# Performance work log

Measured on AMD Instinct MI355X. Metric: run time of the kernel, lower is better.

Reference implementation:

```python
import jax, jax.numpy as jnp
import numpy as np

EPS = 1e-06

def _feature_map(x):
    # elu(x) + 1, positive feature map
    return jax.nn.elu(x) + 1.0

def setup_inputs() -> dict:
    key = jax.random.key(0)
    k1, k2, k3 = jax.random.split(key, 3)
    B, L, d_k, d_v = 2, 4096, 128, 128
    Q = jax.random.normal(k1, (B, L, d_k), dtype=jnp.float32)
    K = jax.random.normal(k2, (B, L, d_k), dtype=jnp.float32)
    V = jax.random.normal(k3, (B, L, d_v), dtype=jnp.float32)
    return {"Q": Q, "K": K, "V": V}

def reference(Q, K, V):
    # Causal linear attention (ELU feature map).
    # out_l = phi(Q_l) @ sum_{j<=l} phi(K_j)^T V_j
    # Z_l   = phi(Q_l) . sum_{j<=l} phi(K_j)
    phiQ = _feature_map(Q)                       # (B, L, dk)
    phiK = _feature_map(K)                       # (B, L, dk)
    # cumulative KV state: (B, L, dk, dv) -- parallel replacement of the
    # original per-step bmm loop
    KV = jnp.cumsum(phiK[..., :, None] * V[..., None, :], axis=1)
    out = jnp.einsum('blk,blkv->blv', phiQ, KV)  # (B, L, dv)
    Kc = jnp.cumsum(phiK, axis=1)                # (B, L, dk)
    Z = jnp.einsum('blk,blk->bl', phiQ, Kc)[..., None]  # (B, L, 1)
    return out / (Z + EPS)
```

## Files before the change

### kernel.cpp

```cpp
#include <hip/hip_runtime.h>


#define EPS 1e-6f

constexpr int Bc = 2;
constexpr int L  = 4096;
constexpr int D  = 128;
constexpr int C  = 128;
constexpr int NC = L / C;
constexpr int P  = 136;

typedef short sh8 __attribute__((ext_vector_type(8)));
typedef float f4  __attribute__((ext_vector_type(4)));

__device__ __forceinline__ float phi(float x) {
    return x > 0.0f ? x + 1.0f : __expf(x);
}
__device__ __forceinline__ unsigned short f2bf(float f) {
    unsigned u = __float_as_uint(f);
    unsigned r = (u + 0x7FFFu + ((u >> 16) & 1u)) >> 16;
    return (unsigned short)r;
}
__device__ __forceinline__ float bf2f(unsigned short h) {
    return __uint_as_float(((unsigned)h) << 16);
}

__global__ __launch_bounds__(256) void k1(
    const float* __restrict__ K, const float* __restrict__ V,
    unsigned short* __restrict__ SB, float* __restrict__ Ksum) {
    const int c = blockIdx.x, b = blockIdx.y, vs = blockIdx.z;
    const int tid = threadIdx.x;
    __shared__ __align__(16) unsigned short sA[64 * P];
    __shared__ __align__(16) unsigned short sB[128 * P];
    const size_t base = ((size_t)b * L + (size_t)c * C) * D;

    for (int k = 0; k < 8; ++k) {
        int fi = tid + 256 * k;
        int l = fi & 127, v4 = fi >> 7;
        float4 vd = *(const float4*)(V + base + (size_t)l * D + vs * 64 + v4 * 4);
        sA[(v4 * 4 + 0) * P + l] = f2bf(vd.x);
        sA[(v4 * 4 + 1) * P + l] = f2bf(vd.y);
        sA[(v4 * 4 + 2) * P + l] = f2bf(vd.z);
        sA[(v4 * 4 + 3) * P + l] = f2bf(vd.w);
    }
    for (int k = 0; k < 16; ++k) {
        int fi = tid + 256 * k;
        int l = fi & 127, i4 = fi >> 7;
        float4 kd = *(const float4*)(K + base + (size_t)l * D + i4 * 4);
        sB[(i4 * 4 + 0) * P + l] = f2bf(phi(kd.x));
        sB[(i4 * 4 + 1) * P + l] = f2bf(phi(kd.y));
        sB[(i4 * 4 + 2) * P + l] = f2bf(phi(kd.z));
        sB[(i4 * 4 + 3) * P + l] = f2bf(phi(kd.w));
    }
    __syncthreads();

    if (vs == 0 && tid < 128) {
        const unsigned* row = (const unsigned*)(sB + tid * P);
        float s = 0.0f;
        for (int j = 0; j < 64; ++j) {
            unsigned d = row[(tid + j) & 63];
            s += bf2f((unsigned short)(d & 0xffff)) + bf2f((unsigned short)(d >> 16));
        }
        Ksum[((size_t)(b * NC + c)) * D + tid] = s;
    }

    const int w = tid >> 6, lane = tid & 63;
    const int r = lane & 15, q = lane >> 4;
    f4 acc[8];
#pragma unroll
    for (int f = 0; f < 8; ++f) acc[f] = {0.f, 0.f, 0.f, 0.f};
#pragma unroll
    for (int ks = 0; ks < 4; ++ks) {
        sh8 a = *(const sh8*)(sA + (w * 16 + r) * P + ks * 32 + q * 8);
#pragma unroll
        for (int f = 0; f < 8; ++f) {
            sh8 bb = *(const sh8*)(sB + (f * 16 + r) * P + ks * 32 + q * 8);
            acc[f] = __builtin_amdgcn_mfma_f32_16x16x32_bf16(a, bb, acc[f], 0, 0, 0);
        }
    }
    unsigned short* out = SB + ((size_t)(b * NC + c)) * D * D;
#pragma unroll
    for (int f = 0; f < 8; ++f) {
        int i = f * 16 + r;
#pragma unroll
        for (int e = 0; e < 4; ++e) {
            int v = vs * 64 + w * 16 + q * 4 + e;
            out[(size_t)v * D + i] = f2bf(acc[f][e]);
        }
    }
}

__global__ __launch_bounds__(256) void k_scan(unsigned short* __restrict__ SB,
                                              float* __restrict__ Ksum) {
    const int SD = D * D;
    int idx = blockIdx.x * 256 + threadIdx.x;
    if (idx < Bc * SD) {
        int b = idx / SD, e = idx % SD;
        float run = 0.0f;
        for (int c = 0; c < NC; ++c) {
            size_t off = ((size_t)(b * NC + c)) * SD + e;
            float t = bf2f(SB[off]);
            SB[off]  = f2bf(run);
            run += t;
        }
    } else if (idx < Bc * SD + Bc * D) {
        int rr = idx - Bc * SD;
        int b = rr >> 7, i = rr & 127;
        float run = 0.0f;
        for (int c = 0; c < NC; ++c) {
            size_t off = ((size_t)(b * NC + c)) * D + i;
            float t = Ksum[off];
            Ksum[off] = run;
            run += t;
        }
    }
}

__global__ __launch_bounds__(256) void k_out(
    const float* __restrict__ Q, const float* __restrict__ K,
    const float* __restrict__ V, const unsigned short* __restrict__ SB,
    const float* __restrict__ Ksum, float* __restrict__ Out) {
    const int c = blockIdx.x, b = blockIdx.y, rs = blockIdx.z;
    const int tid = threadIdx.x;
    __shared__ __align__(16) unsigned short sQ[32 * P];
    __shared__ __align__(16) unsigned short sB[128 * P];
    __shared__ __align__(16) unsigned short sAm[32 * P];
    __shared__ float sKp[128];
    __shared__ float sZ[32];
    const size_t base  = ((size_t)b * L + (size_t)c * C) * D;
    const size_t qbase = base + (size_t)rs * 32 * D;

    for (int k = 0; k < 4; ++k) {
        int fi = tid + 256 * k;
        int row = fi >> 5, c4 = fi & 31;
        float4 qd = *(const float4*)(Q + qbase + (size_t)row * D + c4 * 4);
        uint2 pk;
        pk.x = (unsigned)f2bf(phi(qd.x)) | ((unsigned)f2bf(phi(qd.y)) << 16);
        pk.y = (unsigned)f2bf(phi(qd.z)) | ((unsigned)f2bf(phi(qd.w)) << 16);
        *(uint2*)(sQ + row * P + c4 * 4) = pk;
    }
    for (int k = 0; k < 16; ++k) {
        int fi = tid + 256 * k;
        int row = fi >> 5, c4 = fi & 31;
        float4 kd = *(const float4*)(K + base + (size_t)row * D + c4 * 4);
        uint2 pk;
        pk.x = (unsigned)f2bf(phi(kd.x)) | ((unsigned)f2bf(phi(kd.y)) << 16);
        pk.y = (unsigned)f2bf(phi(kd.z)) | ((unsigned)f2bf(phi(kd.w)) << 16);
        *(uint2*)(sB + row * P + c4 * 4) = pk;
    }
    if (tid < 128) sKp[tid] = Ksum[((size_t)(b * NC + c)) * D + tid];
    __syncthreads();

    const int w = tid >> 6, lane = tid & 63;
    const int r = lane & 15, q = lane >> 4;
    const int rbase = (w & 1) * 16;
    const int cbase = (w >> 1) * 64;

    f4 a2[4];
#pragma unroll
    for (int f = 0; f < 4; ++f) a2[f] = {0.f, 0.f, 0.f, 0.f};
#pragma unroll
    for (int ks = 0; ks < 4; ++ks) {
        sh8 a = *(const sh8*)(sQ + (rbase + r) * P + ks * 32 + q * 8);
#pragma unroll
        for (int f = 0; f < 4; ++f) {
            sh8 bb = *(const sh8*)(sB + (cbase + f * 16 + r) * P + ks * 32 + q * 8);
            a2[f] = __builtin_amdgcn_mfma_f32_16x16x32_bf16(a, bb, a2[f], 0, 0, 0);
        }
    }
#pragma unroll
    for (int f = 0; f < 4; ++f) {
        int j = cbase + f * 16 + r;
#pragma unroll
        for (int e = 0; e < 4; ++e) {
            int lr = rbase + q * 4 + e;
            float vv = (j <= rs * 32 + lr) ? a2[f][e] : 0.0f;
            sAm[lr * P + j] = f2bf(vv);
        }
    }
    __syncthreads();

    for (int k = 0; k < 16; ++k) {
        int fi = tid + 256 * k;
        int j = fi & 127, v4 = fi >> 7;
        float4 vd = *(const float4*)(V + base + (size_t)j * D + v4 * 4);
        sB[(v4 * 4 + 0) * P + j] = f2bf(vd.x);
        sB[(v4 * 4 + 1) * P + j] = f2bf(vd.y);
        sB[(v4 * 4 + 2) * P + j] = f2bf(vd.z);
        sB[(v4 * 4 + 3) * P + j] = f2bf(vd.w);
    }
    if (tid < 32) {
        const unsigned* am = (const unsigned*)(sAm + tid * P);
        const unsigned* qq = (const unsigned*)(sQ + tid * P);
        float zi = 0.0f, zn = 0.0f;
        for (int j = 0; j < 64; ++j) {
            int jj = (tid + j) & 63;
            unsigned da = am[jj];
            zi += bf2f((unsigned short)(da & 0xffff)) + bf2f((unsigned short)(da >> 16));
            unsigned dq = qq[jj];
            zn += bf2f((unsigned short)(dq & 0xffff)) * sKp[2 * jj]
                + bf2f((unsigned short)(dq >> 16))    * sKp[2 * jj + 1];
        }
        sZ[tid] = zi + zn + EPS;
    }
    __syncthreads();

    f4 acc[4];
#pragma unroll
    for (int f = 0; f < 4; ++f) acc[f] = {0.f, 0.f, 0.f, 0.f};
#pragma unroll
    for (int ks = 0; ks < 4; ++ks) {
        sh8 a = *(const sh8*)(sAm + (rbase + r) * P + ks * 32 + q * 8);
#pragma unroll
        for (int f = 0; f < 4; ++f) {
            sh8 bb = *(const sh8*)(sB + (cbase + f * 16 + r) * P + ks * 32 + q * 8);
            acc[f] = __builtin_amdgcn_mfma_f32_16x16x32_bf16(a, bb, acc[f], 0, 0, 0);
        }
    }
    __syncthreads();

    const uint4* sbg = (const uint4*)(SB + ((size_t)(b * NC + c)) * D * D);
    for (int k = 0; k < 8; ++k) {
        int fi = tid + 256 * k;
        int v = fi >> 4, ch = fi & 15;
        uint4 dd = sbg[fi];
        *(uint4*)(sB + v * P + ch * 8) = dd;
    }
    __syncthreads();

#pragma unroll
    for (int ks = 0; ks < 4; ++ks) {
        sh8 a = *(const sh8*)(sQ + (rbase + r) * P + ks * 32 + q * 8);
#pragma unroll
        for (int f = 0; f < 4; ++f) {
            sh8 bb = *(const sh8*)(sB + (cbase + f * 16 + r) * P + ks * 32 + q * 8);
            acc[f] = __builtin_amdgcn_mfma_f32_16x16x32_bf16(a, bb, acc[f], 0, 0, 0);
        }
    }

#pragma unroll
    for (int f = 0; f < 4; ++f) {
        int v = cbase + f * 16 + r;
#pragma unroll
        for (int e = 0; e < 4; ++e) {
            int lr = rbase + q * 4 + e;
            Out[base + (size_t)(rs * 32 + lr) * D + v] = acc[f][e] / sZ[lr];
        }
    }
}

extern "C" void kernel_launch(void* const* d_in, const int* in_sizes, int n_in,
                              void* d_out, int out_size, void* d_ws, size_t ws_size,
                              hipStream_t stream) {
    const float* Q = (const float*)d_in[0];
    const float* K = (const float*)d_in[1];
    const float* V = (const float*)d_in[2];
    float* Out = (float*)d_out;
    unsigned short* SB = (unsigned short*)d_ws;
    float* Ksum = (float*)((char*)d_ws + (size_t)Bc * NC * D * D * 2);

    k1<<<dim3(NC, Bc, 2), 256, 0, stream>>>(K, V, SB, Ksum);
    int total = Bc * D * D + Bc * D;
    k_scan<<<dim3((total + 255) / 256), 256, 0, stream>>>(SB, Ksum);
    k_out<<<dim3(NC, Bc, 4), 256, 0, stream>>>(Q, K, V, SB, Ksum, Out);
}
```

Before: 84.13 us.

## Fold K-sum and normalizer reductions into MFMA via ones-row augmentation, use 512 threads

Instead of summing rows serially with a few threads, both kernels append a row of ones (and the prefix K-sum row) to the shared operand tiles, so the normalizer and K-sums come out of extra MFMA tiles computed by designated waves. Blocks grow to 512 threads with each wave owning a smaller output tile, and k_out loads V up front into a separate buffer, removing a barrier and a serialized reload phase. This trades more shared memory per block, and K-sum and Z now computed with bf16 operands (Ksum rounded to bf16), for removal of the single-thread reduction loops.

```diff
diff --git a/kernel.cpp b/kernel.cpp
--- a/kernel.cpp
+++ b/kernel.cpp
@@ -18,24 +18,23 @@
 }
 __device__ __forceinline__ unsigned short f2bf(float f) {
     unsigned u = __float_as_uint(f);
-    unsigned r = (u + 0x7FFFu + ((u >> 16) & 1u)) >> 16;
-    return (unsigned short)r;
+    return (unsigned short)((u + 0x7FFFu + ((u >> 16) & 1u)) >> 16);
 }
 __device__ __forceinline__ float bf2f(unsigned short h) {
     return __uint_as_float(((unsigned)h) << 16);
 }
 
-__global__ __launch_bounds__(256) void k1(
+__global__ __launch_bounds__(512) void k1(
     const float* __restrict__ K, const float* __restrict__ V,
     unsigned short* __restrict__ SB, float* __restrict__ Ksum) {
     const int c = blockIdx.x, b = blockIdx.y, vs = blockIdx.z;
     const int tid = threadIdx.x;
-    __shared__ __align__(16) unsigned short sA[64 * P];
-    __shared__ __align__(16) unsigned short sB[128 * P];
+    __shared__ __align__(16) unsigned short sA[80 * P];
+    __shared__ __align__(16) unsigned short sKb[128 * P];
     const size_t base = ((size_t)b * L + (size_t)c * C) * D;
 
-    for (int k = 0; k < 8; ++k) {
-        int fi = tid + 256 * k;
+    for (int k = 0; k < 4; ++k) {
+        int fi = tid + 512 * k;
         int l = fi & 127, v4 = fi >> 7;
         float4 vd = *(const float4*)(V + base + (size_t)l * D + vs * 64 + v4 * 4);
         sA[(v4 * 4 + 0) * P + l] = f2bf(vd.x);
@@ -43,50 +42,56 @@
         sA[(v4 * 4 + 2) * P + l] = f2bf(vd.z);
         sA[(v4 * 4 + 3) * P + l] = f2bf(vd.w);
     }
-    for (int k = 0; k < 16; ++k) {
-        int fi = tid + 256 * k;
+    for (int k = 0; k < 2; ++k) {
+        int fi = tid + 512 * k;
+        int row = fi >> 6, colp = fi & 63;
+        *(unsigned*)(sA + (64 + row) * P + colp * 2) = (row == 0) ? 0x3F803F80u : 0u;
+    }
+    for (int k = 0; k < 8; ++k) {
+        int fi = tid + 512 * k;
         int l = fi & 127, i4 = fi >> 7;
         float4 kd = *(const float4*)(K + base + (size_t)l * D + i4 * 4);
-        sB[(i4 * 4 + 0) * P + l] = f2bf(phi(kd.x));
-        sB[(i4 * 4 + 1) * P + l] = f2bf(phi(kd.y));
-        sB[(i4 * 4 + 2) * P + l] = f2bf(phi(kd.z));
-        sB[(i4 * 4 + 3) * P + l] = f2bf(phi(kd.w));
-    }
-    __syncthreads();
-
-    if (vs == 0 && tid < 128) {
-        const unsigned* row = (const unsigned*)(sB + tid * P);
-        float s = 0.0f;
-        for (int j = 0; j < 64; ++j) {
-            unsigned d = row[(tid + j) & 63];
-            s += bf2f((unsigned short)(d & 0xffff)) + bf2f((unsigned short)(d >> 16));
-        }
-        Ksum[((size_t)(b * NC + c)) * D + tid] = s;
-    }
+        sKb[(i4 * 4 + 0) * P + l] = f2bf(phi(kd.x));
+        sKb[(i4 * 4 + 1) * P + l] = f2bf(phi(kd.y));
+        sKb[(i4 * 4 + 2) * P + l] = f2bf(phi(kd.z));
+        sKb[(i4 * 4 + 3) * P + l] = f2bf(phi(kd.w));
+    }
+    __syncthreads();
 
     const int w = tid >> 6, lane = tid & 63;
     const int r = lane & 15, q = lane >> 4;
-    f4 acc[8];
-#pragma unroll
-    for (int f = 0; f < 8; ++f) acc[f] = {0.f, 0.f, 0.f, 0.f};
-#pragma unroll
-    for (int ks = 0; ks < 4; ++ks) {
-        sh8 a = *(const sh8*)(sA + (w * 16 + r) * P + ks * 32 + q * 8);
-#pragma unroll
-        for (int f = 0; f < 8; ++f) {
-            sh8 bb = *(const sh8*)(sB + (f * 16 + r) * P + ks * 32 + q * 8);
+    const int rbase = (w & 3) * 16;
+    const int cbase = (w >> 2) * 64;
+    const bool doZ = (vs == 0) && ((w & 3) == 0);
+
+    f4 acc[4], kz[4];
+#pragma unroll
+    for (int f = 0; f < 4; ++f) { acc[f] = {0.f,0.f,0.f,0.f}; kz[f] = {0.f,0.f,0.f,0.f}; }
+#pragma unroll
+    for (int ks = 0; ks < 4; ++ks) {
+        sh8 a  = *(const sh8*)(sA + (rbase + r) * P + ks * 32 + q * 8);
+        sh8 az = *(const sh8*)(sA + (64 + r) * P + ks * 32 + q * 8);
+#pragma unroll
+        for (int f = 0; f < 4; ++f) {
+            sh8 bb = *(const sh8*)(sKb + (cbase + f * 16 + r) * P + ks * 32 + q * 8);
             acc[f] = __builtin_amdgcn_mfma_f32_16x16x32_bf16(a, bb, acc[f], 0, 0, 0);
+            if (doZ) kz[f] = __builtin_amdgcn_mfma_f32_16x16x32_bf16(az, bb, kz[f], 0, 0, 0);
         }
     }
     unsigned short* out = SB + ((size_t)(b * NC + c)) * D * D;
 #pragma unroll
-    for (int f = 0; f < 8; ++f) {
-        int i = f * 16 + r;
+    for (int f = 0; f < 4; ++f) {
+        int i = cbase + f * 16 + r;
 #pragma unroll
         for (int e = 0; e < 4; ++e) {
-            int v = vs * 64 + w * 16 + q * 4 + e;
+            int v = vs * 64 + rbase + q * 4 + e;
             out[(size_t)v * D + i] = f2bf(acc[f][e]);
         }
+    }
+    if (doZ && q == 0) {
+#pragma unroll
+        for (int f = 0; f < 4; ++f)
+            Ksum[((size_t)(b * NC + c)) * D + cbase + f * 16 + r] = kz[f][0];
     }
 }
 
@@ -116,22 +121,22 @@
     }
 }
 
-__global__ __launch_bounds__(256) void k_out(
+__global__ __launch_bounds__(512) void k_out(
     const float* __restrict__ Q, const float* __restrict__ K,
     const float* __restrict__ V, const unsigned short* __restrict__ SB,
     const float* __restrict__ Ksum, float* __restrict__ Out) {
     const int c = blockIdx.x, b = blockIdx.y, rs = blockIdx.z;
     const int tid = threadIdx.x;
     __shared__ __align__(16) unsigned short sQ[32 * P];
-    __shared__ __align__(16) unsigned short sB[128 * P];
+    __shared__ __align__(16) unsigned short sKb[144 * P];
+    __shared__ __align__(16) unsigned short sV[144 * P];
     __shared__ __align__(16) unsigned short sAm[32 * P];
-    __shared__ float sKp[128];
     __shared__ float sZ[32];
     const size_t base  = ((size_t)b * L + (size_t)c * C) * D;
     const size_t qbase = base + (size_t)rs * 32 * D;
 
-    for (int k = 0; k < 4; ++k) {
-        int fi = tid + 256 * k;
+    for (int k = 0; k < 2; ++k) {
+        int fi = tid + 512 * k;
         int row = fi >> 5, c4 = fi & 31;
         float4 qd = *(const float4*)(Q + qbase + (size_t)row * D + c4 * 4);
         uint2 pk;
@@ -139,92 +144,99 @@
         pk.y = (unsigned)f2bf(phi(qd.z)) | ((unsigned)f2bf(phi(qd.w)) << 16);
         *(uint2*)(sQ + row * P + c4 * 4) = pk;
     }
-    for (int k = 0; k < 16; ++k) {
-        int fi = tid + 256 * k;
+    for (int k = 0; k < 8; ++k) {
+        int fi = tid + 512 * k;
         int row = fi >> 5, c4 = fi & 31;
         float4 kd = *(const float4*)(K + base + (size_t)row * D + c4 * 4);
         uint2 pk;
         pk.x = (unsigned)f2bf(phi(kd.x)) | ((unsigned)f2bf(phi(kd.y)) << 16);
         pk.y = (unsigned)f2bf(phi(kd.z)) | ((unsigned)f2bf(phi(kd.w)) << 16);
-        *(uint2*)(sB + row * P + c4 * 4) = pk;
-    }
-    if (tid < 128) sKp[tid] = Ksum[((size_t)(b * NC + c)) * D + tid];
+        *(uint2*)(sKb + row * P + c4 * 4) = pk;
+    }
+    for (int k = 0; k < 8; ++k) {
+        int fi = tid + 512 * k;
+        int j = fi & 127, v4 = fi >> 7;
+        float4 vd = *(const float4*)(V + base + (size_t)j * D + v4 * 4);
+        sV[(v4 * 4 + 0) * P + j] = f2bf(vd.x);
+        sV[(v4 * 4 + 1) * P + j] = f2bf(vd.y);
+        sV[(v4 * 4 + 2) * P + j] = f2bf(vd.z);
+        sV[(v4 * 4 + 3) * P + j] = f2bf(vd.w);
+    }
+    for (int k = 0; k < 2; ++k) {
+        int fi = tid + 512 * k;
+        int row = fi >> 6, colp = fi & 63;
+        *(unsigned*)(sV + (128 + row) * P + colp * 2) = (row == 0) ? 0x3F803F80u : 0u;
+    }
     __syncthreads();
 
     const int w = tid >> 6, lane = tid & 63;
     const int r = lane & 15, q = lane >> 4;
     const int rbase = (w & 1) * 16;
-    const int cbase = (w >> 1) * 64;
-
-    f4 a2[4];
-#pragma unroll
-    for (int f = 0; f < 4; ++f) a2[f] = {0.f, 0.f, 0.f, 0.f};
+    const int cq = w >> 1, cbase = cq * 32;
+    const bool doZ = (cq == 3);
+
+    f4 a2[2];
+#pragma unroll
+    for (int f = 0; f < 2; ++f) a2[f] = {0.f,0.f,0.f,0.f};
 #pragma unroll
     for (int ks = 0; ks < 4; ++ks) {
         sh8 a = *(const sh8*)(sQ + (rbase + r) * P + ks * 32 + q * 8);
 #pragma unroll
-        for (int f = 0; f < 4; ++f) {
-            sh8 bb = *(const sh8*)(sB + (cbase + f * 16 + r) * P + ks * 32 + q * 8);
+        for (int f = 0; f < 2; ++f) {
+            sh8 bb = *(const sh8*)(sKb + (cbase + f * 16 + r) * P + ks * 32 + q * 8);
             a2[f] = __builtin_amdgcn_mfma_f32_16x16x32_bf16(a, bb, a2[f], 0, 0, 0);
         }
     }
 #pragma unroll
-    for (int f = 0; f < 4; ++f) {
+    for (int f = 0; f < 2; ++f) {
         int j = cbase + f * 16 + r;
 #pragma unroll
         for (int e = 0; e < 4; ++e) {
             int lr = rbase + q * 4 + e;
-            float vv = (j <= rs * 32 + lr) ? a2[f][e] : 0.0f;
-            sAm[lr * P + j] = f2bf(vv);
-        }
-    }
-    __syncthreads();
-
-    for (int k = 0; k < 16; ++k) {
-        int fi = tid + 256 * k;
-        int j = fi & 127, v4 = fi >> 7;
-        float4 vd = *(const float4*)(V + base + (size_t)j * D + v4 * 4);
-        sB[(v4 * 4 + 0) * P + j] = f2bf(vd.x);
-        sB[(v4 * 4 + 1) * P + j] = f2bf(vd.y);
-        sB[(v4 * 4 + 2) * P + j] = f2bf(vd.z);
-        sB[(v4 * 4 + 3) * P + j] = f2bf(vd.w);
-    }
-    if (tid < 32) {
-        const unsigned* am = (const unsigned*)(sAm + tid * P);
-        const unsigned* qq = (const unsigned*)(sQ + tid * P);
-        float zi = 0.0f, zn = 0.0f;
-        for (int j = 0; j < 64; ++j) {
-            int jj = (tid + j) & 63;
-            unsigned da = am[jj];
-            zi += bf2f((unsigned short)(da & 0xffff)) + bf2f((unsigned short)(da >> 16));
-            unsigned dq = qq[jj];
-            zn += bf2f((unsigned short)(dq & 0xffff)) * sKp[2 * jj]
-                + bf2f((unsigned short)(dq >> 16))    * sKp[2 * jj + 1];
-        }
-        sZ[tid] = zi + zn + EPS;
-    }
-    __syncthreads();
-
-    f4 acc[4];
-#pragma unroll
-    for (int f = 0; f < 4; ++f) acc[f] = {0.f, 0.f, 0.f, 0.f};
+            sAm[lr * P + j] = f2bf((j <= rs * 32 + lr) ? a2[f][e] : 0.0f);
+        }
+    }
+    __syncthreads();
+
+    {
+        const uint4* sbg = (const uint4*)(SB + ((size_t)(b * NC + c)) * D * D);
+        for (int k = 0; k < 4; ++k) {
+            int fi = tid + 512 * k;
+            int v = fi >> 4, ch = fi & 15;
+            uint4 dd = sbg[fi];
+            *(uint4*)(sKb + v * P + ch * 8) = dd;
+        }
+        if (tid < 32) {
+            float4 kq = ((const float4*)(Ksum + ((size_t)(b * NC + c)) * D))[tid];
+            uint2 pk;
+            pk.x = (unsigned)f2bf(kq.x) | ((unsigned)f2bf(kq.y) << 16);
+            pk.y = (unsigned)f2bf(kq.z) | ((unsigned)f2bf(kq.w) << 16);
+            *(uint2*)(sKb + 128 * P + tid * 4) = pk;
+        }
+        for (int k = 0; k < 2; ++k) {
+            int fi = tid + 512 * k;
+            if (fi < 960) {
+                int row = 129 + (fi >> 6), colp = fi & 63;
+                *(unsigned*)(sKb + row * P + colp * 2) = 0u;
+            }
+        }
+    }
+
+    f4 acc[2], zacc = {0.f,0.f,0.f,0.f};
+#pragma unroll
+    for (int f = 0; f < 2; ++f) acc[f] = {0.f,0.f,0.f,0.f};
 #pragma unroll
     for (int ks = 0; ks < 4; ++ks) {
         sh8 a = *(const sh8*)(sAm + (rbase + r) * P + ks * 32 + q * 8);
 #pragma unroll
-        for (int f = 0; f < 4; ++f) {
-            sh8 bb = *(const sh8*)(sB + (cbase + f * 16 + r) * P + ks * 32 + q * 8);
+        for (int f = 0; f < 2; ++f) {
+            sh8 bb = *(const sh8*)(sV + (cbase + f * 16 + r) * P + ks * 32 + q * 8);
             acc[f] = __builtin_amdgcn_mfma_f32_16x16x32_bf16(a, bb, acc[f], 0, 0, 0);
         }
-    }
-    __syncthreads();
-
-    const uint4* sbg = (const uint4*)(SB + ((size_t)(b * NC + c)) * D * D);
-    for (int k = 0; k < 8; ++k) {
-        int fi = tid + 256 * k;
-        int v = fi >> 4, ch = fi & 15;
-        uint4 dd = sbg[fi];
-        *(uint4*)(sB + v * P + ch * 8) = dd;
+        if (doZ) {
+            sh8 bz = *(const sh8*)(sV + (128 + r) * P + ks * 32 + q * 8);
+            zacc = __builtin_amdgcn_mfma_f32_16x16x32_bf16(a, bz, zacc, 0, 0, 0);
+        }
     }
     __syncthreads();
 
@@ -232,14 +244,23 @@
     for (int ks = 0; ks < 4; ++ks) {
         sh8 a = *(const sh8*)(sQ + (rbase + r) * P + ks * 32 + q * 8);
 #pragma unroll
-        for (int f = 0; f < 4; ++f) {
-            sh8 bb = *(const sh8*)(sB + (cbase + f * 16 + r) * P + ks * 32 + q * 8);
+        for (int f = 0; f < 2; ++f) {
+            sh8 bb = *(const sh8*)(sKb + (cbase + f * 16 + r) * P + ks * 32 + q * 8);
             acc[f] = __builtin_amdgcn_mfma_f32_16x16x32_bf16(a, bb, acc[f], 0, 0, 0);
         }
-    }
-
-#pragma unroll
-    for (int f = 0; f < 4; ++f) {
+        if (doZ) {
+            sh8 bz = *(const sh8*)(sKb + (128 + r) * P + ks * 32 + q * 8);
+            zacc = __builtin_amdgcn_mfma_f32_16x16x32_bf16(a, bz, zacc, 0, 0, 0);
+        }
+    }
+    if (doZ && r == 0) {
+#pragma unroll
+        for (int e = 0; e < 4; ++e) sZ[rbase + q * 4 + e] = zacc[e] + EPS;
+    }
+    __syncthreads();
+
+#pragma unroll
+    for (int f = 0; f < 2; ++f) {
         int v = cbase + f * 16 + r;
 #pragma unroll
         for (int e = 0; e < 4; ++e) {
@@ -256,11 +277,11 @@
     const float* K = (const float*)d_in[1];
     const float* V = (const float*)d_in[2];
     float* Out = (float*)d_out;
-    unsigned short* SB = (unsigned short*)d_ws;
+    unsigned short* SBw = (unsigned short*)d_ws;
     float* Ksum = (float*)((char*)d_ws + (size_t)Bc * NC * D * D * 2);
 
-    k1<<<dim3(NC, Bc, 2), 256, 0, stream>>>(K, V, SB, Ksum);
+    k1<<<dim3(NC, Bc, 2), 512, 0, stream>>>(K, V, SBw, Ksum);
     int total = Bc * D * D + Bc * D;
-    k_scan<<<dim3((total + 255) / 256), 256, 0, stream>>>(SB, Ksum);
-    k_out<<<dim3(NC, Bc, 4), 256, 0, stream>>>(Q, K, V, SB, Ksum, Out);
-}
+    k_scan<<<dim3((total + 255) / 256), 256, 0, stream>>>(SBw, Ksum);
+    k_out<<<dim3(NC, Bc, 4), 512, 0, stream>>>(Q, K, V, SBw, Ksum, Out);
+}
```

Measured after the change: 80.67 us. 1.04x faster.

## Fuse chunk-state, scan and output into one cooperative kernel with grid sync

Applied to the files above, without the earlier changes.

Replaces the three launches (chunk KV state, serial scan, output) with one cooperative kernel of 64 blocks of 512 threads. Each block computes its chunk state, writes it to the workspace, waits at a grid-wide barrier, then sums the states of all earlier chunks itself instead of running a separate scan. The K-sum and normaliser are computed with MFMA against a ones vector instead of scalar loops, and Q, K and V are loaded once per block. In exchange it relies on cooperative launch and does redundant prefix reads, up to 31 earlier chunk states per block, with only 64 blocks resident.

```diff
diff --git a/kernel.cpp b/kernel.cpp
--- a/kernel.cpp
+++ b/kernel.cpp
@@ -1,4 +1,5 @@
 #include <hip/hip_runtime.h>
+#include <hip/hip_cooperative_groups.h>
 
 
 #define EPS 1e-6f
@@ -18,235 +19,256 @@
 }
 __device__ __forceinline__ unsigned short f2bf(float f) {
     unsigned u = __float_as_uint(f);
-    unsigned r = (u + 0x7FFFu + ((u >> 16) & 1u)) >> 16;
-    return (unsigned short)r;
-}
-__device__ __forceinline__ float bf2f(unsigned short h) {
-    return __uint_as_float(((unsigned)h) << 16);
-}
-
-__global__ __launch_bounds__(256) void k1(
-    const float* __restrict__ K, const float* __restrict__ V,
-    unsigned short* __restrict__ SB, float* __restrict__ Ksum) {
-    const int c = blockIdx.x, b = blockIdx.y, vs = blockIdx.z;
+    return (unsigned short)((u + 0x7FFFu + ((u >> 16) & 1u)) >> 16);
+}
+__device__ __forceinline__ unsigned packbf(float a, float b) {
+    return (unsigned)f2bf(a) | ((unsigned)f2bf(b) << 16);
+}
+__device__ __forceinline__ sh8 splat1() {
+    sh8 s;
+#pragma unroll
+    for (int j = 0; j < 8; ++j) s[j] = (short)0x3F80;
+    return s;
+}
+
+__global__ __launch_bounds__(512) void k_fused(
+    const float* __restrict__ Q, const float* __restrict__ K,
+    const float* __restrict__ V, unsigned short* __restrict__ aggS,
+    float* __restrict__ aggK, float* __restrict__ Out) {
+    const int c = blockIdx.x, b = blockIdx.y;
     const int tid = threadIdx.x;
-    __shared__ __align__(16) unsigned short sA[64 * P];
-    __shared__ __align__(16) unsigned short sB[128 * P];
+    __shared__ __align__(16) unsigned short sQ[128 * P];
+    __shared__ __align__(16) unsigned short sK[128 * P];
+    __shared__ __align__(16) unsigned short sKT[128 * P];
+    __shared__ __align__(16) unsigned short sVT[128 * P];
+    __shared__ float sKp[128];
+    __shared__ float sZ[128];
+    unsigned short* sAm = sKT;
+    unsigned short* sS  = sVT;
+
     const size_t base = ((size_t)b * L + (size_t)c * C) * D;
 
     for (int k = 0; k < 8; ++k) {
-        int fi = tid + 256 * k;
-        int l = fi & 127, v4 = fi >> 7;
-        float4 vd = *(const float4*)(V + base + (size_t)l * D + vs * 64 + v4 * 4);
-        sA[(v4 * 4 + 0) * P + l] = f2bf(vd.x);
-        sA[(v4 * 4 + 1) * P + l] = f2bf(vd.y);
-        sA[(v4 * 4 + 2) * P + l] = f2bf(vd.z);
-        sA[(v4 * 4 + 3) * P + l] = f2bf(vd.w);
-    }
-    for (int k = 0; k < 16; ++k) {
-        int fi = tid + 256 * k;
-        int l = fi & 127, i4 = fi >> 7;
+        int fi = tid + 512 * k;
+        int l = fi >> 5, i4 = fi & 31;
+        float4 qd = *(const float4*)(Q + base + (size_t)l * D + i4 * 4);
         float4 kd = *(const float4*)(K + base + (size_t)l * D + i4 * 4);
-        sB[(i4 * 4 + 0) * P + l] = f2bf(phi(kd.x));
-        sB[(i4 * 4 + 1) * P + l] = f2bf(phi(kd.y));
-        sB[(i4 * 4 + 2) * P + l] = f2bf(phi(kd.z));
-        sB[(i4 * 4 + 3) * P + l] = f2bf(phi(kd.w));
-    }
-    __syncthreads();
-
-    if (vs == 0 && tid < 128) {
-        const unsigned* row = (const unsigned*)(sB + tid * P);
-        float s = 0.0f;
-        for (int j = 0; j < 64; ++j) {
-            unsigned d = row[(tid + j) & 63];
-            s += bf2f((unsigned short)(d & 0xffff)) + bf2f((unsigned short)(d >> 16));
-        }
-        Ksum[((size_t)(b * NC + c)) * D + tid] = s;
-    }
+        float4 vd = *(const float4*)(V + base + (size_t)l * D + i4 * 4);
+        uint2 pq; pq.x = packbf(phi(qd.x), phi(qd.y)); pq.y = packbf(phi(qd.z), phi(qd.w));
+        *(uint2*)(sQ + l * P + i4 * 4) = pq;
+        unsigned short k0 = f2bf(phi(kd.x)), k1 = f2bf(phi(kd.y));
+        unsigned short k2 = f2bf(phi(kd.z)), k3 = f2bf(phi(kd.w));
+        uint2 pk; pk.x = (unsigned)k0 | ((unsigned)k1 << 16); pk.y = (unsigned)k2 | ((unsigned)k3 << 16);
+        *(uint2*)(sK + l * P + i4 * 4) = pk;
+        int blk = (((l >> 3) + i4) & 15) * 8 + (l & 7);
+        sKT[(i4 * 4 + 0) * P + blk] = k0;
+        sKT[(i4 * 4 + 1) * P + blk] = k1;
+        sKT[(i4 * 4 + 2) * P + blk] = k2;
+        sKT[(i4 * 4 + 3) * P + blk] = k3;
+        sVT[(i4 * 4 + 0) * P + blk] = f2bf(vd.x);
+        sVT[(i4 * 4 + 1) * P + blk] = f2bf(vd.y);
+        sVT[(i4 * 4 + 2) * P + blk] = f2bf(vd.z);
+        sVT[(i4 * 4 + 3) * P + blk] = f2bf(vd.w);
+    }
+    __syncthreads();
 
     const int w = tid >> 6, lane = tid & 63;
     const int r = lane & 15, q = lane >> 4;
-    f4 acc[8];
+    const int rowb = (w & 3) * 32;
+    const int wc = w >> 2, colb = wc * 64;
+    const bool doK = ((w & 3) == 0);
+    const bool doZ = (wc == 0);
+
+    {
+        f4 s1[8], kz[4];
+#pragma unroll
+        for (int f = 0; f < 8; ++f) s1[f] = {0.f, 0.f, 0.f, 0.f};
+#pragma unroll
+        for (int f = 0; f < 4; ++f) kz[f] = {0.f, 0.f, 0.f, 0.f};
+        const sh8 ones = splat1();
+#pragma unroll
+        for (int ks = 0; ks < 4; ++ks) {
+            int kq = ks * 4 + q;
+            int vr0 = rowb + r, vr1 = rowb + 16 + r;
+            sh8 a0 = *(const sh8*)(sVT + vr0 * P + ((kq + (vr0 >> 2)) & 15) * 8);
+            sh8 a1 = *(const sh8*)(sVT + vr1 * P + ((kq + (vr1 >> 2)) & 15) * 8);
+#pragma unroll
+            for (int f = 0; f < 4; ++f) {
+                int ir = colb + f * 16 + r;
+                sh8 bk = *(const sh8*)(sKT + ir * P + ((kq + (ir >> 2)) & 15) * 8);
+                s1[f]     = __builtin_amdgcn_mfma_f32_16x16x32_bf16(a0, bk, s1[f], 0, 0, 0);
+                s1[4 + f] = __builtin_amdgcn_mfma_f32_16x16x32_bf16(a1, bk, s1[4 + f], 0, 0, 0);
+                if (doK) kz[f] = __builtin_amdgcn_mfma_f32_16x16x32_bf16(ones, bk, kz[f], 0, 0, 0);
+            }
+        }
+        unsigned short* ag = aggS + ((size_t)(b * NC + c)) * D * D;
+#pragma unroll
+        for (int fr = 0; fr < 2; ++fr)
+#pragma unroll
+            for (int f = 0; f < 4; ++f) {
+                int i = colb + f * 16 + r;
+#pragma unroll
+                for (int e = 0; e < 4; ++e) {
+                    int v = rowb + fr * 16 + q * 4 + e;
+                    ag[(size_t)v * D + i] = f2bf(s1[fr * 4 + f][e]);
+                }
+            }
+        if (doK && q == 0) {
+#pragma unroll
+            for (int f = 0; f < 4; ++f)
+                aggK[((size_t)(b * NC + c)) * D + colb + f * 16 + r] = kz[f][0];
+        }
+    }
+    __threadfence();
+    cooperative_groups::this_grid().sync();
+
+    float pr[32];
+#pragma unroll
+    for (int t = 0; t < 32; ++t) pr[t] = 0.f;
+    if (tid < 128) {
+        float s = 0.f;
+        for (int j = 0; j < c; ++j) s += aggK[((size_t)(b * NC + j)) * D + tid];
+        sKp[tid] = s;
+    }
+    {
+        const unsigned short* ab = aggS + (size_t)b * NC * D * D;
+        for (int j = 0; j < c; ++j) {
+            const uint4* p = (const uint4*)(ab + (size_t)j * D * D) + tid * 4;
+            uint4 dd[4] = {p[0], p[1], p[2], p[3]};
+#pragma unroll
+            for (int a = 0; a < 4; ++a) {
+                unsigned uu[4] = {dd[a].x, dd[a].y, dd[a].z, dd[a].w};
+#pragma unroll
+                for (int u = 0; u < 4; ++u) {
+                    int e0 = a * 8 + u * 2;
+                    pr[e0]     += __uint_as_float(uu[u] << 16);
+                    pr[e0 + 1] += __uint_as_float(uu[u] & 0xFFFF0000u);
+                }
+            }
+        }
+    }
+
+    {
+        f4 a2[8];
+#pragma unroll
+        for (int f = 0; f < 8; ++f) a2[f] = {0.f, 0.f, 0.f, 0.f};
+#pragma unroll
+        for (int ks = 0; ks < 4; ++ks) {
+            sh8 aq0 = *(const sh8*)(sQ + (rowb + r) * P + ks * 32 + q * 8);
+            sh8 aq1 = *(const sh8*)(sQ + (rowb + 16 + r) * P + ks * 32 + q * 8);
+#pragma unroll
+            for (int f = 0; f < 4; ++f) {
+                sh8 bk = *(const sh8*)(sK + (colb + f * 16 + r) * P + ks * 32 + q * 8);
+                a2[f]     = __builtin_amdgcn_mfma_f32_16x16x32_bf16(aq0, bk, a2[f], 0, 0, 0);
+                a2[4 + f] = __builtin_amdgcn_mfma_f32_16x16x32_bf16(aq1, bk, a2[4 + f], 0, 0, 0);
+            }
+        }
+#pragma unroll
+        for (int fr = 0; fr < 2; ++fr)
+#pragma unroll
+            for (int f = 0; f < 4; ++f) {
+                int j = colb + f * 16 + r;
+#pragma unroll
+                for (int e = 0; e < 4; ++e) {
+                    int l = rowb + fr * 16 + q * 4 + e;
+                    sAm[l * P + j] = f2bf((j <= l) ? a2[fr * 4 + f][e] : 0.f);
+                }
+            }
+    }
+    __syncthreads();
+
+    f4 acc[8], z3[2];
 #pragma unroll
     for (int f = 0; f < 8; ++f) acc[f] = {0.f, 0.f, 0.f, 0.f};
-#pragma unroll
-    for (int ks = 0; ks < 4; ++ks) {
-        sh8 a = *(const sh8*)(sA + (w * 16 + r) * P + ks * 32 + q * 8);
-#pragma unroll
-        for (int f = 0; f < 8; ++f) {
-            sh8 bb = *(const sh8*)(sB + (f * 16 + r) * P + ks * 32 + q * 8);
-            acc[f] = __builtin_amdgcn_mfma_f32_16x16x32_bf16(a, bb, acc[f], 0, 0, 0);
-        }
-    }
-    unsigned short* out = SB + ((size_t)(b * NC + c)) * D * D;
-#pragma unroll
-    for (int f = 0; f < 8; ++f) {
-        int i = f * 16 + r;
-#pragma unroll
-        for (int e = 0; e < 4; ++e) {
-            int v = vs * 64 + w * 16 + q * 4 + e;
-            out[(size_t)v * D + i] = f2bf(acc[f][e]);
-        }
-    }
-}
-
-__global__ __launch_bounds__(256) void k_scan(unsigned short* __restrict__ SB,
-                                              float* __restrict__ Ksum) {
-    const int SD = D * D;
-    int idx = blockIdx.x * 256 + threadIdx.x;
-    if (idx < Bc * SD) {
-        int b = idx / SD, e = idx % SD;
-        float run = 0.0f;
-        for (int c = 0; c < NC; ++c) {
-            size_t off = ((size_t)(b * NC + c)) * SD + e;
-            float t = bf2f(SB[off]);
-            SB[off]  = f2bf(run);
-            run += t;
-        }
-    } else if (idx < Bc * SD + Bc * D) {
-        int rr = idx - Bc * SD;
-        int b = rr >> 7, i = rr & 127;
-        float run = 0.0f;
-        for (int c = 0; c < NC; ++c) {
-            size_t off = ((size_t)(b * NC + c)) * D + i;
-            float t = Ksum[off];
-            Ksum[off] = run;
-            run += t;
-        }
-    }
-}
-
-__global__ __launch_bounds__(256) void k_out(
-    const float* __restrict__ Q, const float* __restrict__ K,
-    const float* __restrict__ V, const unsigned short* __restrict__ SB,
-    const float* __restrict__ Ksum, float* __restrict__ Out) {
-    const int c = blockIdx.x, b = blockIdx.y, rs = blockIdx.z;
-    const int tid = threadIdx.x;
-    __shared__ __align__(16) unsigned short sQ[32 * P];
-    __shared__ __align__(16) unsigned short sB[128 * P];
-    __shared__ __align__(16) unsigned short sAm[32 * P];
-    __shared__ float sKp[128];
-    __shared__ float sZ[32];
-    const size_t base  = ((size_t)b * L + (size_t)c * C) * D;
-    const size_t qbase = base + (size_t)rs * 32 * D;
-
-    for (int k = 0; k < 4; ++k) {
-        int fi = tid + 256 * k;
-        int row = fi >> 5, c4 = fi & 31;
-        float4 qd = *(const float4*)(Q + qbase + (size_t)row * D + c4 * 4);
-        uint2 pk;
-        pk.x = (unsigned)f2bf(phi(qd.x)) | ((unsigned)f2bf(phi(qd.y)) << 16);
-        pk.y = (unsigned)f2bf(phi(qd.z)) | ((unsigned)f2bf(phi(qd.w)) << 16);
-        *(uint2*)(sQ + row * P + c4 * 4) = pk;
-    }
-    for (int k = 0; k < 16; ++k) {
-        int fi = tid + 256 * k;
-        int row = fi >> 5, c4 = fi & 31;
-        float4 kd = *(const float4*)(K + base + (size_t)row * D + c4 * 4);
-        uint2 pk;
-        pk.x = (unsigned)f2bf(phi(kd.x)) | ((unsigned)f2bf(phi(kd.y)) << 16);
-        pk.y = (unsigned)f2bf(phi(kd.z)) | ((unsigned)f2bf(phi(kd.w)) << 16);
-        *(uint2*)(sB + row * P + c4 * 4) = pk;
-    }
-    if (tid < 128) sKp[tid] = Ksum[((size_t)(b * NC + c)) * D + tid];
-    __syncthreads();
-
-    const int w = tid >> 6, lane = tid & 63;
-    const int r = lane & 15, q = lane >> 4;
-    const int rbase = (w & 1) * 16;
-    const int cbase = (w >> 1) * 64;
-
-    f4 a2[4];
-#pragma unroll
-    for (int f = 0; f < 4; ++f) a2[f] = {0.f, 0.f, 0.f, 0.f};
-#pragma unroll
-    for (int ks = 0; ks < 4; ++ks) {
-        sh8 a = *(const sh8*)(sQ + (rbase + r) * P + ks * 32 + q * 8);
+    z3[0] = {0.f, 0.f, 0.f, 0.f}; z3[1] = {0.f, 0.f, 0.f, 0.f};
+    {
+        const sh8 ones = splat1();
+#pragma unroll
+        for (int ks = 0; ks < 4; ++ks) {
+            int kq = ks * 4 + q;
+            sh8 am0 = *(const sh8*)(sAm + (rowb + r) * P + ks * 32 + q * 8);
+            sh8 am1 = *(const sh8*)(sAm + (rowb + 16 + r) * P + ks * 32 + q * 8);
+#pragma unroll
+            for (int f = 0; f < 4; ++f) {
+                int vr = colb + f * 16 + r;
+                sh8 bv = *(const sh8*)(sVT + vr * P + ((kq + (vr >> 2)) & 15) * 8);
+                acc[f]     = __builtin_amdgcn_mfma_f32_16x16x32_bf16(am0, bv, acc[f], 0, 0, 0);
+                acc[4 + f] = __builtin_amdgcn_mfma_f32_16x16x32_bf16(am1, bv, acc[4 + f], 0, 0, 0);
+            }
+            if (doZ) {
+                z3[0] = __builtin_amdgcn_mfma_f32_16x16x32_bf16(am0, ones, z3[0], 0, 0, 0);
+                z3[1] = __builtin_amdgcn_mfma_f32_16x16x32_bf16(am1, ones, z3[1], 0, 0, 0);
+            }
+        }
+    }
+    __syncthreads();
+
+    {
+        int vr = tid >> 2, i0 = (tid & 3) * 32;
+        unsigned short* dst = sS + vr * P + i0;
+#pragma unroll
+        for (int a = 0; a < 4; ++a) {
+            uint4 o;
+            o.x = packbf(pr[a * 8 + 0], pr[a * 8 + 1]);
+            o.y = packbf(pr[a * 8 + 2], pr[a * 8 + 3]);
+            o.z = packbf(pr[a * 8 + 4], pr[a * 8 + 5]);
+            o.w = packbf(pr[a * 8 + 6], pr[a * 8 + 7]);
+            *(uint4*)(dst + a * 8) = o;
+        }
+    }
+    __syncthreads();
+
+    {
+        sh8 bzk[4];
+        if (doZ) {
+#pragma unroll
+            for (int ks = 0; ks < 4; ++ks) {
+                float4 f0 = *(const float4*)(sKp + ks * 32 + q * 8);
+                float4 f1 = *(const float4*)(sKp + ks * 32 + q * 8 + 4);
+                sh8 t;
+                t[0] = (short)f2bf(f0.x); t[1] = (short)f2bf(f0.y);
+                t[2] = (short)f2bf(f0.z); t[3] = (short)f2bf(f0.w);
+                t[4] = (short)f2bf(f1.x); t[5] = (short)f2bf(f1.y);
+                t[6] = (short)f2bf(f1.z); t[7] = (short)f2bf(f1.w);
+                bzk[ks] = t;
+            }
+        }
+#pragma unroll
+        for (int ks = 0; ks < 4; ++ks) {
+            sh8 aq0 = *(const sh8*)(sQ + (rowb + r) * P + ks * 32 + q * 8);
+            sh8 aq1 = *(const sh8*)(sQ + (rowb + 16 + r) * P + ks * 32 + q * 8);
+#pragma unroll
+            for (int f = 0; f < 4; ++f) {
+                sh8 bs = *(const sh8*)(sS + (colb + f * 16 + r) * P + ks * 32 + q * 8);
+                acc[f]     = __builtin_amdgcn_mfma_f32_16x16x32_bf16(aq0, bs, acc[f], 0, 0, 0);
+                acc[4 + f] = __builtin_amdgcn_mfma_f32_16x16x32_bf16(aq1, bs, acc[4 + f], 0, 0, 0);
+            }
+            if (doZ) {
+                z3[0] = __builtin_amdgcn_mfma_f32_16x16x32_bf16(aq0, bzk[ks], z3[0], 0, 0, 0);
+                z3[1] = __builtin_amdgcn_mfma_f32_16x16x32_bf16(aq1, bzk[ks], z3[1], 0, 0, 0);
+            }
+        }
+        if (doZ && r == 0) {
+#pragma unroll
+            for (int fr = 0; fr < 2; ++fr)
+#pragma unroll
+                for (int e = 0; e < 4; ++e)
+                    sZ[rowb + fr * 16 + q * 4 + e] = z3[fr][e] + EPS;
+        }
+    }
+    __syncthreads();
+
+#pragma unroll
+    for (int fr = 0; fr < 2; ++fr)
 #pragma unroll
         for (int f = 0; f < 4; ++f) {
-            sh8 bb = *(const sh8*)(sB + (cbase + f * 16 + r) * P + ks * 32 + q * 8);
-            a2[f] = __builtin_amdgcn_mfma_f32_16x16x32_bf16(a, bb, a2[f], 0, 0, 0);
-        }
-    }
-#pragma unroll
-    for (int f = 0; f < 4; ++f) {
-        int j = cbase + f * 16 + r;
-#pragma unroll
-        for (int e = 0; e < 4; ++e) {
-            int lr = rbase + q * 4 + e;
-            float vv = (j <= rs * 32 + lr) ? a2[f][e] : 0.0f;
-            sAm[lr * P + j] = f2bf(vv);
-        }
-    }
-    __syncthreads();
-
-    for (int k = 0; k < 16; ++k) {
-        int fi = tid + 256 * k;
-        int j = fi & 127, v4 = fi >> 7;
-        float4 vd = *(const float4*)(V + base + (size_t)j * D + v4 * 4);
-        sB[(v4 * 4 + 0) * P + j] = f2bf(vd.x);
-        sB[(v4 * 4 + 1) * P + j] = f2bf(vd.y);
-        sB[(v4 * 4 + 2) * P + j] = f2bf(vd.z);
-        sB[(v4 * 4 + 3) * P + j] = f2bf(vd.w);
-    }
-    if (tid < 32) {
-        const unsigned* am = (const unsigned*)(sAm + tid * P);
-        const unsigned* qq = (const unsigned*)(sQ + tid * P);
-        float zi = 0.0f, zn = 0.0f;
-        for (int j = 0; j < 64; ++j) {
-            int jj = (tid + j) & 63;
-            unsigned da = am[jj];
-            zi += bf2f((unsigned short)(da & 0xffff)) + bf2f((unsigned short)(da >> 16));
-            unsigned dq = qq[jj];
-            zn += bf2f((unsigned short)(dq & 0xffff)) * sKp[2 * jj]
-                + bf2f((unsigned short)(dq >> 16))    * sKp[2 * jj + 1];
-        }
-        sZ[tid] = zi + zn + EPS;
-    }
-    __syncthreads();
-
-    f4 acc[4];
-#pragma unroll
-    for (int f = 0; f < 4; ++f) acc[f] = {0.f, 0.f, 0.f, 0.f};
-#pragma unroll
-    for (int ks = 0; ks < 4; ++ks) {
-        sh8 a = *(const sh8*)(sAm + (rbase + r) * P + ks * 32 + q * 8);
-#pragma unroll
-        for (int f = 0; f < 4; ++f) {
-            sh8 bb = *(const sh8*)(sB + (cbase + f * 16 + r) * P + ks * 32 + q * 8);
-            acc[f] = __builtin_amdgcn_mfma_f32_16x16x32_bf16(a, bb, acc[f], 0, 0, 0);
-        }
-    }
-    __syncthreads();
-
-    const uint4* sbg = (const uint4*)(SB + ((size_t)(b * NC + c)) * D * D);
-    for (int k = 0; k < 8; ++k) {
-        int fi = tid + 256 * k;
-        int v = fi >> 4, ch = fi & 15;
-        uint4 dd = sbg[fi];
-        *(uint4*)(sB + v * P + ch * 8) = dd;
-    }
-    __syncthreads();
-
-#pragma unroll
-    for (int ks = 0; ks < 4; ++ks) {
-        sh8 a = *(const sh8*)(sQ + (rbase + r) * P + ks * 32 + q * 8);
-#pragma unroll
-        for (int f = 0; f < 4; ++f) {
-            sh8 bb = *(const sh8*)(sB + (cbase + f * 16 + r) * P + ks * 32 + q * 8);
-            acc[f] = __builtin_amdgcn_mfma_f32_16x16x32_bf16(a, bb, acc[f], 0, 0, 0);
-        }
-    }
-
-#pragma unroll
-    for (int f = 0; f < 4; ++f) {
-        int v = cbase + f * 16 + r;
-#pragma unroll
-        for (int e = 0; e < 4; ++e) {
-            int lr = rbase + q * 4 + e;
-            Out[base + (size_t)(rs * 32 + lr) * D + v] = acc[f][e] / sZ[lr];
-        }
-    }
+            int v = colb + f * 16 + r;
+#pragma unroll
+            for (int e = 0; e < 4; ++e) {
+                int l = rowb + fr * 16 + q * 4 + e;
+                Out[base + (size_t)l * D + v] = acc[fr * 4 + f][e] / sZ[l];
+            }
+        }
 }
 
 extern "C" void kernel_launch(void* const* d_in, const int* in_sizes, int n_in,
@@ -256,11 +278,11 @@
     const float* K = (const float*)d_in[1];
     const float* V = (const float*)d_in[2];
     float* Out = (float*)d_out;
-    unsigned short* SB = (unsigned short*)d_ws;
-    float* Ksum = (float*)((char*)d_ws + (size_t)Bc * NC * D * D * 2);
-
-    k1<<<dim3(NC, Bc, 2), 256, 0, stream>>>(K, V, SB, Ksum);
-    int total = Bc * D * D + Bc * D;
-    k_scan<<<dim3((total + 255) / 256), 256, 0, stream>>>(SB, Ksum);
-    k_out<<<dim3(NC, Bc, 4), 256, 0, stream>>>(Q, K, V, SB, Ksum, Out);
-}
+    unsigned short* aggS = (unsigned short*)d_ws;
+    float* aggK = (float*)((char*)d_ws + (size_t)Bc * NC * D * D * 2);
+
+    void* args[] = {(void*)&Q, (void*)&K, (void*)&V,
+                    (void*)&aggS, (void*)&aggK, (void*)&Out};
+    hipLaunchCooperativeKernel((const void*)k_fused, dim3(NC, Bc), dim3(512),
+                               args, 0, stream);
+}
```

Result: slower. 137.7 us (+63.6%).
